# Optimization experiments

Hardware: AMD Instinct MI355X
Metric: run time of the kernel (lower is better)

The kernel has to match this reference:

```python
import jax, jax.numpy as jnp
import numpy as np

HEADS = 8


def setup_inputs() -> dict:
    key = jax.random.key(0)
    ks = jax.random.split(key, 7)
    B, C, H, W = 8, 512, 64, 64
    K, MEM = 64, 512
    s = 0.02
    return {
        "x": jax.random.normal(ks[0], (B, C, H, W), dtype=jnp.float32),
        "Ft": jax.random.normal(ks[1], (B, K, MEM), dtype=jnp.float32),
        "Wq": jax.random.normal(ks[2], (C, C), dtype=jnp.float32) * s,
        "Wk": jax.random.normal(ks[3], (C, MEM), dtype=jnp.float32) * s,
        "Wv": jax.random.normal(ks[4], (C, MEM), dtype=jnp.float32) * s,
        "Wp": jax.random.normal(ks[5], (C, C), dtype=jnp.float32) * s,
        "bp": jax.random.normal(ks[6], (C,), dtype=jnp.float32) * s,
    }


def reference(x, Ft, Wq, Wk, Wv, Wp, bp):
    B, C, H, W = x.shape
    h = HEADS
    d = C // h
    N = H * W
    # 1x1 conv query projection: (out_c, in_c) applied over spatial dims
    q = jnp.einsum('oc,bchw->bohw', Wq, x).reshape(B, h, d, N)
    q = jnp.transpose(q, (0, 1, 3, 2))                      # [B,h,N,d]
    # Linear K/V on memory tokens: Ft [B,K,MEM] @ W^T -> [B,K,C]
    k = (Ft @ Wk.T).reshape(B, -1, h, d).transpose(0, 2, 1, 3)  # [B,h,K,d]
    v = (Ft @ Wv.T).reshape(B, -1, h, d).transpose(0, 2, 1, 3)  # [B,h,K,d]
    attn = jnp.einsum('bhnc,bhkc->bhnk', q, k) / jnp.sqrt(jnp.float32(d))
    attn = jax.nn.softmax(attn, axis=-1)
    out = jnp.einsum('bhnk,bhkc->bhnc', attn, v)            # [B,h,N,d]
    out = jnp.transpose(out, (0, 1, 3, 2)).reshape(B, C, H, W)
    out = jnp.einsum('oc,bchw->bohw', Wp, out) + bp[None, :, None, None]
    return x + out
```

## Files before the change

### kernel.cpp

```cpp
#include <hip/hip_runtime.h>
#include <cstdint>
#include <cstddef>

#define BATCH 8
#define CDIM  512
#define NPIX  4096
#define NHEAD 8
#define DH    64
#define KTOK  64
#define MEM   512

#define BK    64

typedef __attribute__((ext_vector_type(8))) short          bf8;
typedef __attribute__((ext_vector_type(4))) float          f4;
typedef __attribute__((ext_vector_type(4))) unsigned short us4;

__device__ __forceinline__ unsigned short f2bf(float f){
  union { float f; unsigned int u; } x; x.f = f;
  unsigned int r = (x.u + 0x7fffu + ((x.u >> 16) & 1u)) >> 16;
  return (unsigned short)r;
}

__device__ __forceinline__ void gld_lds16(const unsigned short* g, unsigned short* lds){
  __builtin_amdgcn_global_load_lds((const __attribute__((address_space(1))) unsigned int*)g,
                                   (__attribute__((address_space(3))) unsigned int*)lds, 16, 0, 0);
}

__global__ __launch_bounds__(256) void wconv(const float* __restrict__ wq, const float* __restrict__ wp,
                                             unsigned short* __restrict__ wqb, unsigned short* __restrict__ wpb){
  int i = (blockIdx.x * 256 + threadIdx.x) * 4;
  float4 a = *(const float4*)(wq + i);
  us4 pa = { f2bf(a.x), f2bf(a.y), f2bf(a.z), f2bf(a.w) };
  *(us4*)(wqb + i) = pa;
  float4 b = *(const float4*)(wp + i);
  us4 pb = { f2bf(b.x), f2bf(b.y), f2bf(b.z), f2bf(b.w) };
  *(us4*)(wpb + i) = pb;
}

__global__ __launch_bounds__(256) void xtrans(const float* __restrict__ x, unsigned short* __restrict__ xb){
  __shared__ __align__(16) unsigned short t[64 * 68];
  int tid = threadIdx.x;
  int n0 = blockIdx.x * 64, c0 = blockIdx.y * 64, b = blockIdx.z;
  const float* xp = x + ((size_t)(b * CDIM + c0)) * NPIX + n0;
#pragma unroll
  for (int it = 0; it < 4; ++it){
    int idx = it * 1024 + tid * 4;
    int cc = idx >> 6, nn = idx & 63;
    float4 v = *(const float4*)(xp + (size_t)cc * NPIX + nn);
    us4 pk = { f2bf(v.x), f2bf(v.y), f2bf(v.z), f2bf(v.w) };
    *(us4*)&t[cc * 68 + nn] = pk;
  }
  __syncthreads();
  unsigned short* op = xb + ((size_t)(b * NPIX + n0)) * CDIM + c0;
#pragma unroll
  for (int it = 0; it < 4; ++it){
    int idx = it * 1024 + tid * 4;
    int nn = idx >> 6, c4 = idx & 63;
    us4 pk = { t[(c4 + 0) * 68 + nn], t[(c4 + 1) * 68 + nn],
               t[(c4 + 2) * 68 + nn], t[(c4 + 3) * 68 + nn] };
    *(us4*)(op + (size_t)nn * CDIM + c4) = pk;
  }
}

__global__ __launch_bounds__(256) void kvproj(const float* __restrict__ Ft, const float* __restrict__ Wk,
                                              const float* __restrict__ Wv, unsigned short* __restrict__ kb,
                                              unsigned short* __restrict__ vt){
  __shared__ float ft[8][MEM];
  int tid = threadIdx.x;
  int cg = blockIdx.x, kk0 = blockIdx.y * 8, b = blockIdx.z;
  const float* fp = Ft + ((size_t)(b * KTOK + kk0)) * MEM;
#pragma unroll
  for (int it = 0; it < 4; ++it){
    int idx = it * 1024 + tid * 4;
    int row = idx >> 9, m = idx & 511;
    *(float4*)&ft[row][m] = *(const float4*)(fp + (size_t)row * MEM + m);
  }
  __syncthreads();
  int kv = tid >> 7, cl = tid & 127;
  int c = cg * 128 + cl;
  const float* wrow = (kv ? Wv : Wk) + (size_t)c * MEM;
  float acc[8] = {0.f,0.f,0.f,0.f,0.f,0.f,0.f,0.f};
  for (int m = 0; m < MEM; m += 4){
    float4 wv4 = *(const float4*)(wrow + m);
#pragma unroll
    for (int kk = 0; kk < 8; ++kk){
      acc[kk] += wv4.x * ft[kk][m] + wv4.y * ft[kk][m+1] + wv4.z * ft[kk][m+2] + wv4.w * ft[kk][m+3];
    }
  }
  int h = c >> 6, dd = c & 63;
  if (kv == 0){
#pragma unroll
    for (int kk = 0; kk < 8; ++kk)
      kb[(((size_t)(b * NHEAD + h)) * KTOK + kk0 + kk) * DH + dd] = f2bf(acc[kk] * 0.125f);
  } else {
#pragma unroll
    for (int kk = 0; kk < 8; ++kk)
      vt[(((size_t)(b * NHEAD + h)) * DH + dd) * KTOK + kk0 + kk] = f2bf(acc[kk]);
  }
}

__global__ __launch_bounds__(256, 3) void qattn(const unsigned short* __restrict__ wqb,
                                                const unsigned short* __restrict__ xb,
                                                const unsigned short* __restrict__ kb,
                                                const unsigned short* __restrict__ vt,
                                                unsigned short* __restrict__ att){
  __shared__ __align__(16) unsigned short ab[16384];
  int tid = threadIdx.x;
  int w = tid >> 6, l = tid & 63;
  int lo = l & 15, hi = l >> 4;
  int n0 = blockIdx.x * 128, o0 = blockIdx.y * 128, b = blockIdx.z;
  int ol = (w >> 1) * 64, nl = (w & 1) * 64;

  f4 z = {0.f, 0.f, 0.f, 0.f};
  f4 accq[4][4];
#pragma unroll
  for (int i = 0; i < 4; ++i)
#pragma unroll
    for (int j = 0; j < 4; ++j) accq[i][j] = z;

  const int lrow = l >> 3;
  const int lcc  = (l & 7) ^ lrow;
  const unsigned short* asrc = wqb + ((size_t)(o0 + w * 8 + lrow)) * CDIM + lcc * 8;
  const unsigned short* bsrc = xb + ((size_t)(b * NPIX + n0 + w * 8 + lrow)) * CDIM + lcc * 8;

  for (int t = 0; t < 8; ++t){
    int kc = t * BK;
#pragma unroll
    for (int j = 0; j < 4; ++j){
      int g = j * 4 + w;
      gld_lds16(asrc + (size_t)j * 32 * CDIM + kc, &ab[g * 512]);
      gld_lds16(bsrc + (size_t)j * 32 * CDIM + kc, &ab[8192 + g * 512]);
    }
    __syncthreads();
#pragma unroll
    for (int ks = 0; ks < 2; ++ks){
      int cc = ks * 4 + hi;
      int sw = ((cc ^ (lo & 7)) << 3);
      bf8 af[4], bfr[4];
#pragma unroll
      for (int fi = 0; fi < 4; ++fi)
        af[fi] = *(const bf8*)&ab[(ol + fi * 16 + lo) * 64 + sw];
#pragma unroll
      for (int fj = 0; fj < 4; ++fj)
        bfr[fj] = *(const bf8*)&ab[8192 + (nl + fj * 16 + lo) * 64 + sw];
#pragma unroll
      for (int fi = 0; fi < 4; ++fi)
#pragma unroll
        for (int fj = 0; fj < 4; ++fj)
          accq[fi][fj] = __builtin_amdgcn_mfma_f32_16x16x32_bf16(af[fi], bfr[fj], accq[fi][fj], 0, 0, 0);
    }
    __syncthreads();
  }

  unsigned short* qt = &ab[w * 4096];
#pragma unroll
  for (int fi = 0; fi < 4; ++fi)
#pragma unroll
    for (int fj = 0; fj < 4; ++fj){
      f4 v = accq[fi][fj];
      us4 pk = { f2bf(v[0]), f2bf(v[1]), f2bf(v[2]), f2bf(v[3]) };
      int row = fj * 16 + lo;
      int col = fi * 16 + hi * 4;
      int cs  = (((col >> 3) ^ (row & 7)) << 3) | (col & 7);
      *(us4*)&qt[row * 64 + cs] = pk;
    }

  int head = blockIdx.y * 2 + (w >> 1);
  const unsigned short* kh = kb + ((size_t)(b * NHEAD + head)) * (KTOK * DH);
  f4 accs[4][4];
#pragma unroll
  for (int i = 0; i < 4; ++i)
#pragma unroll
    for (int j = 0; j < 4; ++j) accs[i][j] = z;
#pragma unroll
  for (int ks = 0; ks < 2; ++ks){
    int sw = (((ks * 4 + hi) ^ (lo & 7)) << 3);
    bf8 ka[4];
#pragma unroll
    for (int fi = 0; fi < 4; ++fi)
      ka[fi] = *(const bf8*)(kh + (fi * 16 + lo) * 64 + ks * 32 + hi * 8);
#pragma unroll
    for (int fj = 0; fj < 4; ++fj){
      bf8 qf = *(const bf8*)&qt[(fj * 16 + lo) * 64 + sw];
#pragma unroll
      for (int fi = 0; fi < 4; ++fi)
        accs[fi][fj] = __builtin_amdgcn_mfma_f32_16x16x32_bf16(ka[fi], qf, accs[fi][fj], 0, 0, 0);
    }
  }

#pragma unroll
  for (int fj = 0; fj < 4; ++fj){
    float mx = accs[0][fj][0];
#pragma unroll
    for (int fi = 0; fi < 4; ++fi)
#pragma unroll
      for (int r = 0; r < 4; ++r) mx = fmaxf(mx, accs[fi][fj][r]);
    mx = fmaxf(mx, __shfl_xor(mx, 16));
    mx = fmaxf(mx, __shfl_xor(mx, 32));
    float sm = 0.f;
#pragma unroll
    for (int fi = 0; fi < 4; ++fi)
#pragma unroll
      for (int r = 0; r < 4; ++r){
        float e = __expf(accs[fi][fj][r] - mx);
        accs[fi][fj][r] = e; sm += e;
      }
    sm += __shfl_xor(sm, 16);
    sm += __shfl_xor(sm, 32);
    float inv = 1.0f / sm;
#pragma unroll
    for (int fi = 0; fi < 4; ++fi){
      us4 pk = { f2bf(accs[fi][fj][0] * inv), f2bf(accs[fi][fj][1] * inv),
                 f2bf(accs[fi][fj][2] * inv), f2bf(accs[fi][fj][3] * inv) };
      int row = fj * 16 + lo;
      int col = fi * 16 + hi * 4;
      int cs  = (((col >> 3) ^ (row & 7)) << 3) | (col & 7);
      *(us4*)&qt[row * 64 + cs] = pk;
    }
  }

  const unsigned short* vh = vt + ((size_t)(b * NHEAD + head)) * (DH * KTOK);
  f4 acco[4][4];
#pragma unroll
  for (int i = 0; i < 4; ++i)
#pragma unroll
    for (int j = 0; j < 4; ++j) acco[i][j] = z;
#pragma unroll
  for (int ks = 0; ks < 2; ++ks){
    int sw = (((ks * 4 + hi) ^ (lo & 7)) << 3);
    bf8 va[4];
#pragma unroll
    for (int fi = 0; fi < 4; ++fi)
      va[fi] = *(const bf8*)(vh + (fi * 16 + lo) * 64 + ks * 32 + hi * 8);
#pragma unroll
    for (int fj = 0; fj < 4; ++fj){
      bf8 pf = *(const bf8*)&qt[(fj * 16 + lo) * 64 + sw];
#pragma unroll
      for (int fi = 0; fi < 4; ++fi)
        acco[fi][fj] = __builtin_amdgcn_mfma_f32_16x16x32_bf16(va[fi], pf, acco[fi][fj], 0, 0, 0);
    }
  }

  unsigned short* op = att + ((size_t)(b * NPIX + n0 + nl)) * CDIM + head * 64;
#pragma unroll
  for (int fi = 0; fi < 4; ++fi)
#pragma unroll
    for (int fj = 0; fj < 4; ++fj){
      f4 v = acco[fi][fj];
      us4 pk = { f2bf(v[0]), f2bf(v[1]), f2bf(v[2]), f2bf(v[3]) };
      *(us4*)(op + (size_t)(fj * 16 + lo) * CDIM + fi * 16 + hi * 4) = pk;
    }
}

__global__ __launch_bounds__(256, 3) void pproj(const unsigned short* __restrict__ wpb,
                                                const unsigned short* __restrict__ att,
                                                const float* __restrict__ x,
                                                const float* __restrict__ bpv,
                                                float* __restrict__ out){
  __shared__ __align__(16) unsigned short ab[16384];
  int tid = threadIdx.x;
  int w = tid >> 6, l = tid & 63;
  int lo = l & 15, hi = l >> 4;
  int n0 = blockIdx.x * 128, o0 = blockIdx.y * 128, b = blockIdx.z;
  int ol = (w >> 1) * 64, nl = (w & 1) * 64;

  f4 z = {0.f, 0.f, 0.f, 0.f};
  f4 acc[4][4];
#pragma unroll
  for (int i = 0; i < 4; ++i)
#pragma unroll
    for (int j = 0; j < 4; ++j) acc[i][j] = z;

  const int lrow = l >> 3;
  const int lcc  = (l & 7) ^ lrow;
  const unsigned short* asrc = wpb + ((size_t)(o0 + w * 8 + lrow)) * CDIM + lcc * 8;
  const unsigned short* bsrc = att + ((size_t)(b * NPIX + n0 + w * 8 + lrow)) * CDIM + lcc * 8;

  for (int t = 0; t < 8; ++t){
    int kc = t * BK;
#pragma unroll
    for (int j = 0; j < 4; ++j){
      int g = j * 4 + w;
      gld_lds16(asrc + (size_t)j * 32 * CDIM + kc, &ab[g * 512]);
      gld_lds16(bsrc + (size_t)j * 32 * CDIM + kc, &ab[8192 + g * 512]);
    }
    __syncthreads();
#pragma unroll
    for (int ks = 0; ks < 2; ++ks){
      int cc = ks * 4 + hi;
      int sw = ((cc ^ (lo & 7)) << 3);
      bf8 af[4], bfr[4];
#pragma unroll
      for (int fi = 0; fi < 4; ++fi)
        af[fi] = *(const bf8*)&ab[(ol + fi * 16 + lo) * 64 + sw];
#pragma unroll
      for (int fj = 0; fj < 4; ++fj)
        bfr[fj] = *(const bf8*)&ab[8192 + (nl + fj * 16 + lo) * 64 + sw];
#pragma unroll
      for (int fi = 0; fi < 4; ++fi)
#pragma unroll
        for (int fj = 0; fj < 4; ++fj)
          acc[fi][fj] = __builtin_amdgcn_mfma_f32_16x16x32_bf16(af[fi], bfr[fj], acc[fi][fj], 0, 0, 0);
    }
    __syncthreads();
  }

#pragma unroll
  for (int fi = 0; fi < 4; ++fi)
#pragma unroll
    for (int fj = 0; fj < 4; ++fj){
      int o = o0 + ol + fi * 16 + hi * 4;
      int n = n0 + nl + fj * 16 + lo;
#pragma unroll
      for (int r = 0; r < 4; ++r){
        size_t idx = ((size_t)(b * CDIM + o + r)) * NPIX + n;
        out[idx] = acc[fi][fj][r] + bpv[o + r] + x[idx];
      }
    }
}

extern "C" void kernel_launch(void* const* d_in, const int* in_sizes, int n_in,
                              void* d_out, int out_size, void* d_ws, size_t ws_size,
                              hipStream_t stream){
  const float* x  = (const float*)d_in[0];
  const float* Ft = (const float*)d_in[1];
  const float* Wq = (const float*)d_in[2];
  const float* Wk = (const float*)d_in[3];
  const float* Wv = (const float*)d_in[4];
  const float* Wp = (const float*)d_in[5];
  const float* bp = (const float*)d_in[6];
  float* out = (float*)d_out;

  char* ws = (char*)d_ws;
  unsigned short* wqb = (unsigned short*)(ws);
  unsigned short* wpb = (unsigned short*)(ws + 524288);
  unsigned short* xb  = (unsigned short*)(ws + 1048576);
  unsigned short* att = (unsigned short*)(ws + 1048576 + 33554432);
  unsigned short* kb  = (unsigned short*)(ws + 1048576 + 2ull * 33554432);
  unsigned short* vt  = (unsigned short*)(ws + 1048576 + 2ull * 33554432 + 524288);

  wconv<<<dim3(256), dim3(256), 0, stream>>>(Wq, Wp, wqb, wpb);
  xtrans<<<dim3(64, 8, 8), dim3(256), 0, stream>>>(x, xb);
  kvproj<<<dim3(4, 8, 8), dim3(256), 0, stream>>>(Ft, Wk, Wv, kb, vt);
  qattn<<<dim3(32, 4, 8), dim3(256), 0, stream>>>(wqb, xb, kb, vt, att);
  pproj<<<dim3(32, 4, 8), dim3(256), 0, stream>>>(wpb, att, x, bp, out);
}
```

Measured before the change: 115.7 us.

## Split Q-projection from attention and double-buffer GEMM LDS staging

Splits the fused Q-projection+attention kernel into a standalone Q GEMM that writes bf16 Q to global memory and a separate attention kernel that reads it back. Both GEMMs now use a BK=32 double-buffered LDS pipeline that prefetches the next tile while computing the current one, and occupancy hints rise from 3 to 4. The attention kernel writes its output in place over the Q buffer. This trades an extra 32 MB round trip of Q plus one more launch for better GEMM overlap and occupancy.

```diff
diff --git a/kernel.cpp b/kernel.cpp
--- a/kernel.cpp
+++ b/kernel.cpp
@@ -9,8 +9,6 @@
 #define DH    64
 #define KTOK  64
 #define MEM   512
-
-#define BK    64
 
 typedef __attribute__((ext_vector_type(8))) short          bf8;
 typedef __attribute__((ext_vector_type(4))) float          f4;
@@ -100,11 +98,44 @@
   }
 }
 
-__global__ __launch_bounds__(256, 3) void qattn(const unsigned short* __restrict__ wqb,
+#define GEMM_PRE(APTR, BPTR)                                                              \
+  const int arow = l >> 2;                                                                \
+  const int achk = (l & 3) ^ (arow & 3);                                                  \
+  const unsigned short* aS = (APTR) + (size_t)(o0 + w * 16 + arow) * CDIM + achk * 8;     \
+  const unsigned short* bS = (BPTR) + ((size_t)(b * NPIX) + n0 + w * 16 + arow) * CDIM + achk * 8;
+
+#define STAGE(p, kc)                                                                      \
+  {                                                                                       \
+    _Pragma("unroll")                                                                     \
+    for (int j = 0; j < 2; ++j){                                                          \
+      gld_lds16(aS + (size_t)j * 64 * CDIM + (kc), &ab[(p) * 8192 + (w + j * 4) * 512]);  \
+      gld_lds16(bS + (size_t)j * 64 * CDIM + (kc), &ab[(p) * 8192 + 4096 + (w + j * 4) * 512]); \
+    }                                                                                     \
+  }
+
+#define GEMM_STEP(p, ACC)                                                                 \
+  {                                                                                       \
+    bf8 af[4], bfr[4];                                                                    \
+    _Pragma("unroll")                                                                     \
+    for (int fi = 0; fi < 4; ++fi){                                                       \
+      int r = ol + fi * 16 + lo;                                                          \
+      af[fi] = *(const bf8*)&ab[(p) * 8192 + r * 32 + ((hi ^ (r & 3)) << 3)];             \
+    }                                                                                     \
+    _Pragma("unroll")                                                                     \
+    for (int fj = 0; fj < 4; ++fj){                                                       \
+      int r = nl + fj * 16 + lo;                                                          \
+      bfr[fj] = *(const bf8*)&ab[(p) * 8192 + 4096 + r * 32 + ((hi ^ (r & 3)) << 3)];     \
+    }                                                                                     \
+    _Pragma("unroll")                                                                     \
+    for (int fi = 0; fi < 4; ++fi)                                                        \
+      _Pragma("unroll")                                                                   \
+      for (int fj = 0; fj < 4; ++fj)                                                      \
+        ACC[fi][fj] = __builtin_amdgcn_mfma_f32_16x16x32_bf16(af[fi], bfr[fj], ACC[fi][fj], 0, 0, 0); \
+  }
+
+__global__ __launch_bounds__(256, 4) void qgemm(const unsigned short* __restrict__ wqb,
                                                 const unsigned short* __restrict__ xb,
-                                                const unsigned short* __restrict__ kb,
-                                                const unsigned short* __restrict__ vt,
-                                                unsigned short* __restrict__ att){
+                                                unsigned short* __restrict__ qb){
   __shared__ __align__(16) unsigned short ab[16384];
   int tid = threadIdx.x;
   int w = tid >> 6, l = tid & 63;
@@ -113,61 +144,52 @@
   int ol = (w >> 1) * 64, nl = (w & 1) * 64;
 
   f4 z = {0.f, 0.f, 0.f, 0.f};
-  f4 accq[4][4];
+  f4 acc[4][4];
 #pragma unroll
   for (int i = 0; i < 4; ++i)
 #pragma unroll
-    for (int j = 0; j < 4; ++j) accq[i][j] = z;
-
-  const int lrow = l >> 3;
-  const int lcc  = (l & 7) ^ lrow;
-  const unsigned short* asrc = wqb + ((size_t)(o0 + w * 8 + lrow)) * CDIM + lcc * 8;
-  const unsigned short* bsrc = xb + ((size_t)(b * NPIX + n0 + w * 8 + lrow)) * CDIM + lcc * 8;
-
-  for (int t = 0; t < 8; ++t){
-    int kc = t * BK;
-#pragma unroll
-    for (int j = 0; j < 4; ++j){
-      int g = j * 4 + w;
-      gld_lds16(asrc + (size_t)j * 32 * CDIM + kc, &ab[g * 512]);
-      gld_lds16(bsrc + (size_t)j * 32 * CDIM + kc, &ab[8192 + g * 512]);
-    }
+    for (int j = 0; j < 4; ++j) acc[i][j] = z;
+
+  GEMM_PRE(wqb, xb)
+
+  STAGE(0, 0)
+  __syncthreads();
+  int cur = 0;
+  for (int t = 0; t < 16; ++t){
+    if (t < 15) STAGE(cur ^ 1, (t + 1) * 32)
+    GEMM_STEP(cur, acc)
     __syncthreads();
-#pragma unroll
-    for (int ks = 0; ks < 2; ++ks){
-      int cc = ks * 4 + hi;
-      int sw = ((cc ^ (lo & 7)) << 3);
-      bf8 af[4], bfr[4];
-#pragma unroll
-      for (int fi = 0; fi < 4; ++fi)
-        af[fi] = *(const bf8*)&ab[(ol + fi * 16 + lo) * 64 + sw];
-#pragma unroll
-      for (int fj = 0; fj < 4; ++fj)
-        bfr[fj] = *(const bf8*)&ab[8192 + (nl + fj * 16 + lo) * 64 + sw];
-#pragma unroll
-      for (int fi = 0; fi < 4; ++fi)
-#pragma unroll
-        for (int fj = 0; fj < 4; ++fj)
-          accq[fi][fj] = __builtin_amdgcn_mfma_f32_16x16x32_bf16(af[fi], bfr[fj], accq[fi][fj], 0, 0, 0);
-    }
-    __syncthreads();
-  }
-
-  unsigned short* qt = &ab[w * 4096];
+    cur ^= 1;
+  }
+
+  unsigned short* op = qb + ((size_t)(b * NPIX) + n0 + nl) * CDIM + o0 + ol;
 #pragma unroll
   for (int fi = 0; fi < 4; ++fi)
 #pragma unroll
     for (int fj = 0; fj < 4; ++fj){
-      f4 v = accq[fi][fj];
+      f4 v = acc[fi][fj];
       us4 pk = { f2bf(v[0]), f2bf(v[1]), f2bf(v[2]), f2bf(v[3]) };
-      int row = fj * 16 + lo;
-      int col = fi * 16 + hi * 4;
-      int cs  = (((col >> 3) ^ (row & 7)) << 3) | (col & 7);
-      *(us4*)&qt[row * 64 + cs] = pk;
-    }
-
-  int head = blockIdx.y * 2 + (w >> 1);
-  const unsigned short* kh = kb + ((size_t)(b * NHEAD + head)) * (KTOK * DH);
+      *(us4*)(op + (size_t)(fj * 16 + lo) * CDIM + fi * 16 + hi * 4) = pk;
+    }
+}
+
+__global__ __launch_bounds__(256, 4) void attn(const unsigned short* __restrict__ qb,
+                                               const unsigned short* __restrict__ kb,
+                                               const unsigned short* __restrict__ vt,
+                                               unsigned short* __restrict__ att){
+  __shared__ __align__(16) unsigned short pb[16384];
+  int tid = threadIdx.x;
+  int w = tid >> 6, l = tid & 63;
+  int lo = l & 15, hi = l >> 4;
+  int n0 = blockIdx.x * 256 + w * 64;
+  int head = blockIdx.y, b = blockIdx.z;
+
+  const unsigned short* qh = qb + ((size_t)(b * NPIX) + n0) * CDIM + head * 64;
+  const unsigned short* kh = kb + (size_t)(b * NHEAD + head) * (KTOK * DH);
+  const unsigned short* vh = vt + (size_t)(b * NHEAD + head) * (DH * KTOK);
+  unsigned short* P = &pb[w * 4096];
+
+  f4 z = {0.f, 0.f, 0.f, 0.f};
   f4 accs[4][4];
 #pragma unroll
   for (int i = 0; i < 4; ++i)
@@ -175,14 +197,13 @@
     for (int j = 0; j < 4; ++j) accs[i][j] = z;
 #pragma unroll
   for (int ks = 0; ks < 2; ++ks){
-    int sw = (((ks * 4 + hi) ^ (lo & 7)) << 3);
     bf8 ka[4];
 #pragma unroll
     for (int fi = 0; fi < 4; ++fi)
       ka[fi] = *(const bf8*)(kh + (fi * 16 + lo) * 64 + ks * 32 + hi * 8);
 #pragma unroll
     for (int fj = 0; fj < 4; ++fj){
-      bf8 qf = *(const bf8*)&qt[(fj * 16 + lo) * 64 + sw];
+      bf8 qf = *(const bf8*)(qh + (size_t)(fj * 16 + lo) * CDIM + ks * 32 + hi * 8);
 #pragma unroll
       for (int fi = 0; fi < 4; ++fi)
         accs[fi][fj] = __builtin_amdgcn_mfma_f32_16x16x32_bf16(ka[fi], qf, accs[fi][fj], 0, 0, 0);
@@ -216,11 +237,10 @@
       int row = fj * 16 + lo;
       int col = fi * 16 + hi * 4;
       int cs  = (((col >> 3) ^ (row & 7)) << 3) | (col & 7);
-      *(us4*)&qt[row * 64 + cs] = pk;
-    }
-  }
-
-  const unsigned short* vh = vt + ((size_t)(b * NHEAD + head)) * (DH * KTOK);
+      *(us4*)&P[row * 64 + cs] = pk;
+    }
+  }
+
   f4 acco[4][4];
 #pragma unroll
   for (int i = 0; i < 4; ++i)
@@ -235,14 +255,14 @@
       va[fi] = *(const bf8*)(vh + (fi * 16 + lo) * 64 + ks * 32 + hi * 8);
 #pragma unroll
     for (int fj = 0; fj < 4; ++fj){
-      bf8 pf = *(const bf8*)&qt[(fj * 16 + lo) * 64 + sw];
+      bf8 pf = *(const bf8*)&P[(fj * 16 + lo) * 64 + sw];
 #pragma unroll
       for (int fi = 0; fi < 4; ++fi)
         acco[fi][fj] = __builtin_amdgcn_mfma_f32_16x16x32_bf16(va[fi], pf, acco[fi][fj], 0, 0, 0);
     }
   }
 
-  unsigned short* op = att + ((size_t)(b * NPIX + n0 + nl)) * CDIM + head * 64;
+  unsigned short* op = att + ((size_t)(b * NPIX) + n0) * CDIM + head * 64;
 #pragma unroll
   for (int fi = 0; fi < 4; ++fi)
 #pragma unroll
@@ -253,7 +273,7 @@
     }
 }
 
-__global__ __launch_bounds__(256, 3) void pproj(const unsigned short* __restrict__ wpb,
+__global__ __launch_bounds__(256, 4) void pproj(const unsigned short* __restrict__ wpb,
                                                 const unsigned short* __restrict__ att,
                                                 const float* __restrict__ x,
                                                 const float* __restrict__ bpv,
@@ -272,38 +292,16 @@
 #pragma unroll
     for (int j = 0; j < 4; ++j) acc[i][j] = z;
 
-  const int lrow = l >> 3;
-  const int lcc  = (l & 7) ^ lrow;
-  const unsigned short* asrc = wpb + ((size_t)(o0 + w * 8 + lrow)) * CDIM + lcc * 8;
-  const unsigned short* bsrc = att + ((size_t)(b * NPIX + n0 + w * 8 + lrow)) * CDIM + lcc * 8;
-
-  for (int t = 0; t < 8; ++t){
-    int kc = t * BK;
-#pragma unroll
-    for (int j = 0; j < 4; ++j){
-      int g = j * 4 + w;
-      gld_lds16(asrc + (size_t)j * 32 * CDIM + kc, &ab[g * 512]);
-      gld_lds16(bsrc + (size_t)j * 32 * CDIM + kc, &ab[8192 + g * 512]);
-    }
+  GEMM_PRE(wpb, att)
+
+  STAGE(0, 0)
+  __syncthreads();
+  int cur = 0;
+  for (int t = 0; t < 16; ++t){
+    if (t < 15) STAGE(cur ^ 1, (t + 1) * 32)
+    GEMM_STEP(cur, acc)
     __syncthreads();
-#pragma unroll
-    for (int ks = 0; ks < 2; ++ks){
-      int cc = ks * 4 + hi;
-      int sw = ((cc ^ (lo & 7)) << 3);
-      bf8 af[4], bfr[4];
-#pragma unroll
-      for (int fi = 0; fi < 4; ++fi)
-        af[fi] = *(const bf8*)&ab[(ol + fi * 16 + lo) * 64 + sw];
-#pragma unroll
-      for (int fj = 0; fj < 4; ++fj)
-        bfr[fj] = *(const bf8*)&ab[8192 + (nl + fj * 16 + lo) * 64 + sw];
-#pragma unroll
-      for (int fi = 0; fi < 4; ++fi)
-#pragma unroll
-        for (int fj = 0; fj < 4; ++fj)
-          acc[fi][fj] = __builtin_amdgcn_mfma_f32_16x16x32_bf16(af[fi], bfr[fj], acc[fi][fj], 0, 0, 0);
-    }
-    __syncthreads();
+    cur ^= 1;
   }
 
 #pragma unroll
@@ -336,13 +334,14 @@
   unsigned short* wqb = (unsigned short*)(ws);
   unsigned short* wpb = (unsigned short*)(ws + 524288);
   unsigned short* xb  = (unsigned short*)(ws + 1048576);
-  unsigned short* att = (unsigned short*)(ws + 1048576 + 33554432);
+  unsigned short* qb  = (unsigned short*)(ws + 1048576 + 33554432);
   unsigned short* kb  = (unsigned short*)(ws + 1048576 + 2ull * 33554432);
   unsigned short* vt  = (unsigned short*)(ws + 1048576 + 2ull * 33554432 + 524288);
 
   wconv<<<dim3(256), dim3(256), 0, stream>>>(Wq, Wp, wqb, wpb);
   xtrans<<<dim3(64, 8, 8), dim3(256), 0, stream>>>(x, xb);
   kvproj<<<dim3(4, 8, 8), dim3(256), 0, stream>>>(Ft, Wk, Wv, kb, vt);
-  qattn<<<dim3(32, 4, 8), dim3(256), 0, stream>>>(wqb, xb, kb, vt, att);
-  pproj<<<dim3(32, 4, 8), dim3(256), 0, stream>>>(wpb, att, x, bp, out);
-}
+  qgemm<<<dim3(32, 4, 8), dim3(256), 0, stream>>>(wqb, xb, qb);
+  attn<<<dim3(16, 8, 8), dim3(256), 0, stream>>>(qb, kb, vt, qb);
+  pproj<<<dim3(32, 4, 8), dim3(256), 0, stream>>>(wpb, qb, x, bp, out);
+}
```

Measured after the change: 132.8 us. 14.7% more time.

## Fuse query projection, attention and output projection into one kernel

Applied to the files above, without the earlier changes.

Merges the qattn and pproj kernels into one 512-thread kernel. Each block covers all 512 output channels for 128 pixels, with one wave per head. The attention output stays in LDS instead of making a 32MB bf16 round trip through global memory, and the separate output-projection launch goes away. In exchange, weights are read directly from global memory with no LDS staging, the grid drops to 256 blocks, and register pressure is high (accq[4][8] plus further accumulators), which risks lower occupancy and spills.

```diff
diff --git a/kernel.cpp b/kernel.cpp
--- a/kernel.cpp
+++ b/kernel.cpp
@@ -9,8 +9,6 @@
 #define DH    64
 #define KTOK  64
 #define MEM   512
-
-#define BK    64
 
 typedef __attribute__((ext_vector_type(8))) short          bf8;
 typedef __attribute__((ext_vector_type(4))) float          f4;
@@ -100,224 +98,197 @@
   }
 }
 
-__global__ __launch_bounds__(256, 3) void qattn(const unsigned short* __restrict__ wqb,
+__global__ __launch_bounds__(512, 2) void fused(const unsigned short* __restrict__ wqb,
+                                                const unsigned short* __restrict__ wpb,
                                                 const unsigned short* __restrict__ xb,
                                                 const unsigned short* __restrict__ kb,
                                                 const unsigned short* __restrict__ vt,
-                                                unsigned short* __restrict__ att){
-  __shared__ __align__(16) unsigned short ab[16384];
+                                                const float* __restrict__ x,
+                                                const float* __restrict__ bpv,
+                                                float* __restrict__ out){
+  __shared__ __align__(16) unsigned short r0[32768];
+  __shared__ __align__(16) unsigned short r1[32768];
   int tid = threadIdx.x;
   int w = tid >> 6, l = tid & 63;
   int lo = l & 15, hi = l >> 4;
-  int n0 = blockIdx.x * 128, o0 = blockIdx.y * 128, b = blockIdx.z;
-  int ol = (w >> 1) * 64, nl = (w & 1) * 64;
+  int n0 = blockIdx.x * 128, b = blockIdx.y;
 
   f4 z = {0.f, 0.f, 0.f, 0.f};
-  f4 accq[4][4];
+
+  f4 accq[4][8];
 #pragma unroll
   for (int i = 0; i < 4; ++i)
 #pragma unroll
-    for (int j = 0; j < 4; ++j) accq[i][j] = z;
-
-  const int lrow = l >> 3;
-  const int lcc  = (l & 7) ^ lrow;
-  const unsigned short* asrc = wqb + ((size_t)(o0 + w * 8 + lrow)) * CDIM + lcc * 8;
-  const unsigned short* bsrc = xb + ((size_t)(b * NPIX + n0 + w * 8 + lrow)) * CDIM + lcc * 8;
+    for (int j = 0; j < 8; ++j) accq[i][j] = z;
+
+  const int srow = l >> 3;
+  const int schk = (l & 7) ^ srow;
+  const unsigned short* bS = xb + ((size_t)(b * NPIX) + n0 + w * 8 + srow) * CDIM + schk * 8;
+  const unsigned short* aQ = wqb + (size_t)(w * 64 + lo) * CDIM + hi * 8;
 
   for (int t = 0; t < 8; ++t){
-    int kc = t * BK;
-#pragma unroll
-    for (int j = 0; j < 4; ++j){
-      int g = j * 4 + w;
-      gld_lds16(asrc + (size_t)j * 32 * CDIM + kc, &ab[g * 512]);
-      gld_lds16(bsrc + (size_t)j * 32 * CDIM + kc, &ab[8192 + g * 512]);
-    }
+    gld_lds16(bS + t * 64, &r0[w * 512]);
+    gld_lds16(bS + (size_t)64 * CDIM + t * 64, &r0[(w + 8) * 512]);
     __syncthreads();
 #pragma unroll
     for (int ks = 0; ks < 2; ++ks){
-      int cc = ks * 4 + hi;
-      int sw = ((cc ^ (lo & 7)) << 3);
-      bf8 af[4], bfr[4];
-#pragma unroll
-      for (int fi = 0; fi < 4; ++fi)
-        af[fi] = *(const bf8*)&ab[(ol + fi * 16 + lo) * 64 + sw];
-#pragma unroll
-      for (int fj = 0; fj < 4; ++fj)
-        bfr[fj] = *(const bf8*)&ab[8192 + (nl + fj * 16 + lo) * 64 + sw];
-#pragma unroll
-      for (int fi = 0; fi < 4; ++fi)
-#pragma unroll
-        for (int fj = 0; fj < 4; ++fj)
+      bf8 af[4], bfr[8];
+#pragma unroll
+      for (int fi = 0; fi < 4; ++fi)
+        af[fi] = *(const bf8*)(aQ + (size_t)fi * 16 * CDIM + t * 64 + ks * 32);
+#pragma unroll
+      for (int fj = 0; fj < 8; ++fj)
+        bfr[fj] = *(const bf8*)&r0[(fj * 16 + lo) * 64 + (((ks * 4 + hi) ^ (lo & 7)) << 3)];
+#pragma unroll
+      for (int fi = 0; fi < 4; ++fi)
+#pragma unroll
+        for (int fj = 0; fj < 8; ++fj)
           accq[fi][fj] = __builtin_amdgcn_mfma_f32_16x16x32_bf16(af[fi], bfr[fj], accq[fi][fj], 0, 0, 0);
     }
     __syncthreads();
   }
 
-  unsigned short* qt = &ab[w * 4096];
-#pragma unroll
-  for (int fi = 0; fi < 4; ++fi)
-#pragma unroll
-    for (int fj = 0; fj < 4; ++fj){
-      f4 v = accq[fi][fj];
-      us4 pk = { f2bf(v[0]), f2bf(v[1]), f2bf(v[2]), f2bf(v[3]) };
-      int row = fj * 16 + lo;
-      int col = fi * 16 + hi * 4;
-      int cs  = (((col >> 3) ^ (row & 7)) << 3) | (col & 7);
-      *(us4*)&qt[row * 64 + cs] = pk;
-    }
-
-  int head = blockIdx.y * 2 + (w >> 1);
-  const unsigned short* kh = kb + ((size_t)(b * NHEAD + head)) * (KTOK * DH);
-  f4 accs[4][4];
-#pragma unroll
-  for (int i = 0; i < 4; ++i)
-#pragma unroll
-    for (int j = 0; j < 4; ++j) accs[i][j] = z;
-#pragma unroll
-  for (int ks = 0; ks < 2; ++ks){
-    int sw = (((ks * 4 + hi) ^ (lo & 7)) << 3);
-    bf8 ka[4];
+  const unsigned short* kh = kb + (size_t)(b * NHEAD + w) * (KTOK * DH);
+  const unsigned short* vh = vt + (size_t)(b * NHEAD + w) * (DH * KTOK);
+  unsigned short* qt = &r0[w * 4096];
+
+#pragma unroll
+  for (int nh = 0; nh < 2; ++nh){
 #pragma unroll
     for (int fi = 0; fi < 4; ++fi)
-      ka[fi] = *(const bf8*)(kh + (fi * 16 + lo) * 64 + ks * 32 + hi * 8);
-#pragma unroll
-    for (int fj = 0; fj < 4; ++fj){
-      bf8 qf = *(const bf8*)&qt[(fj * 16 + lo) * 64 + sw];
-#pragma unroll
-      for (int fi = 0; fi < 4; ++fi)
-        accs[fi][fj] = __builtin_amdgcn_mfma_f32_16x16x32_bf16(ka[fi], qf, accs[fi][fj], 0, 0, 0);
-    }
-  }
-
-#pragma unroll
-  for (int fj = 0; fj < 4; ++fj){
-    float mx = accs[0][fj][0];
+#pragma unroll
+      for (int fjl = 0; fjl < 4; ++fjl){
+        f4 v = accq[fi][nh * 4 + fjl];
+        us4 pk = { f2bf(v[0]), f2bf(v[1]), f2bf(v[2]), f2bf(v[3]) };
+        int row = fjl * 16 + lo;
+        int col = fi * 16 + hi * 4;
+        int cs  = (((col >> 3) ^ (row & 7)) << 3) | (col & 7);
+        *(us4*)&qt[row * 64 + cs] = pk;
+      }
+
+    f4 accs[4][4];
+#pragma unroll
+    for (int i = 0; i < 4; ++i)
+#pragma unroll
+      for (int j = 0; j < 4; ++j) accs[i][j] = z;
+#pragma unroll
+    for (int ks = 0; ks < 2; ++ks){
+      bf8 ka[4];
+#pragma unroll
+      for (int fi = 0; fi < 4; ++fi)
+        ka[fi] = *(const bf8*)(kh + (fi * 16 + lo) * 64 + ks * 32 + hi * 8);
+#pragma unroll
+      for (int fjl = 0; fjl < 4; ++fjl){
+        bf8 qf = *(const bf8*)&qt[(fjl * 16 + lo) * 64 + (((ks * 4 + hi) ^ (lo & 7)) << 3)];
+#pragma unroll
+        for (int fi = 0; fi < 4; ++fi)
+          accs[fi][fjl] = __builtin_amdgcn_mfma_f32_16x16x32_bf16(ka[fi], qf, accs[fi][fjl], 0, 0, 0);
+      }
+    }
+
+#pragma unroll
+    for (int fjl = 0; fjl < 4; ++fjl){
+      float mx = accs[0][fjl][0];
+#pragma unroll
+      for (int fi = 0; fi < 4; ++fi)
+#pragma unroll
+        for (int r = 0; r < 4; ++r) mx = fmaxf(mx, accs[fi][fjl][r]);
+      mx = fmaxf(mx, __shfl_xor(mx, 16));
+      mx = fmaxf(mx, __shfl_xor(mx, 32));
+      float sm = 0.f;
+#pragma unroll
+      for (int fi = 0; fi < 4; ++fi)
+#pragma unroll
+        for (int r = 0; r < 4; ++r){
+          float e = __expf(accs[fi][fjl][r] - mx);
+          accs[fi][fjl][r] = e; sm += e;
+        }
+      sm += __shfl_xor(sm, 16);
+      sm += __shfl_xor(sm, 32);
+      float inv = 1.0f / sm;
+#pragma unroll
+      for (int fi = 0; fi < 4; ++fi){
+        us4 pk = { f2bf(accs[fi][fjl][0] * inv), f2bf(accs[fi][fjl][1] * inv),
+                   f2bf(accs[fi][fjl][2] * inv), f2bf(accs[fi][fjl][3] * inv) };
+        int row = fjl * 16 + lo;
+        int col = fi * 16 + hi * 4;
+        int cs  = (((col >> 3) ^ (row & 7)) << 3) | (col & 7);
+        *(us4*)&qt[row * 64 + cs] = pk;
+      }
+    }
+
+    f4 acco[4][4];
+#pragma unroll
+    for (int i = 0; i < 4; ++i)
+#pragma unroll
+      for (int j = 0; j < 4; ++j) acco[i][j] = z;
+#pragma unroll
+    for (int ks = 0; ks < 2; ++ks){
+      int sw = (((ks * 4 + hi) ^ (lo & 7)) << 3);
+      bf8 va[4];
+#pragma unroll
+      for (int fi = 0; fi < 4; ++fi)
+        va[fi] = *(const bf8*)(vh + (fi * 16 + lo) * 64 + ks * 32 + hi * 8);
+#pragma unroll
+      for (int fjl = 0; fjl < 4; ++fjl){
+        bf8 pf = *(const bf8*)&qt[(fjl * 16 + lo) * 64 + sw];
+#pragma unroll
+        for (int fi = 0; fi < 4; ++fi)
+          acco[fi][fjl] = __builtin_amdgcn_mfma_f32_16x16x32_bf16(va[fi], pf, acco[fi][fjl], 0, 0, 0);
+      }
+    }
+
+    __syncthreads();
 #pragma unroll
     for (int fi = 0; fi < 4; ++fi)
 #pragma unroll
-      for (int r = 0; r < 4; ++r) mx = fmaxf(mx, accs[fi][fj][r]);
-    mx = fmaxf(mx, __shfl_xor(mx, 16));
-    mx = fmaxf(mx, __shfl_xor(mx, 32));
-    float sm = 0.f;
+      for (int fjl = 0; fjl < 4; ++fjl){
+        f4 v = acco[fi][fjl];
+        us4 pk = { f2bf(v[0]), f2bf(v[1]), f2bf(v[2]), f2bf(v[3]) };
+        int row = fjl * 16 + lo;
+        int cc  = w * 8 + fi * 2 + (hi >> 1);
+        *(us4*)&r1[row * 512 + ((cc ^ (row & 7)) << 3) + (hi & 1) * 4] = pk;
+      }
+    __syncthreads();
+
+    f4 accp[4][4];
+#pragma unroll
+    for (int i = 0; i < 4; ++i)
+#pragma unroll
+      for (int j = 0; j < 4; ++j) accp[i][j] = z;
+    const unsigned short* aP = wpb + (size_t)(w * 64 + lo) * CDIM + hi * 8;
+#pragma unroll
+    for (int t = 0; t < 8; ++t){
+#pragma unroll
+      for (int ks = 0; ks < 2; ++ks){
+        bf8 pa[4], bt[4];
+#pragma unroll
+        for (int fi = 0; fi < 4; ++fi)
+          pa[fi] = *(const bf8*)(aP + (size_t)fi * 16 * CDIM + t * 64 + ks * 32);
+#pragma unroll
+        for (int fjl = 0; fjl < 4; ++fjl)
+          bt[fjl] = *(const bf8*)&r1[(fjl * 16 + lo) * 512 + (((t * 8 + ks * 4 + hi) ^ (lo & 7)) << 3)];
+#pragma unroll
+        for (int fi = 0; fi < 4; ++fi)
+#pragma unroll
+          for (int fjl = 0; fjl < 4; ++fjl)
+            accp[fi][fjl] = __builtin_amdgcn_mfma_f32_16x16x32_bf16(pa[fi], bt[fjl], accp[fi][fjl], 0, 0, 0);
+      }
+    }
+
 #pragma unroll
     for (int fi = 0; fi < 4; ++fi)
 #pragma unroll
-      for (int r = 0; r < 4; ++r){
-        float e = __expf(accs[fi][fj][r] - mx);
-        accs[fi][fj][r] = e; sm += e;
-      }
-    sm += __shfl_xor(sm, 16);
-    sm += __shfl_xor(sm, 32);
-    float inv = 1.0f / sm;
-#pragma unroll
-    for (int fi = 0; fi < 4; ++fi){
-      us4 pk = { f2bf(accs[fi][fj][0] * inv), f2bf(accs[fi][fj][1] * inv),
-                 f2bf(accs[fi][fj][2] * inv), f2bf(accs[fi][fj][3] * inv) };
-      int row = fj * 16 + lo;
-      int col = fi * 16 + hi * 4;
-      int cs  = (((col >> 3) ^ (row & 7)) << 3) | (col & 7);
-      *(us4*)&qt[row * 64 + cs] = pk;
-    }
-  }
-
-  const unsigned short* vh = vt + ((size_t)(b * NHEAD + head)) * (DH * KTOK);
-  f4 acco[4][4];
-#pragma unroll
-  for (int i = 0; i < 4; ++i)
-#pragma unroll
-    for (int j = 0; j < 4; ++j) acco[i][j] = z;
-#pragma unroll
-  for (int ks = 0; ks < 2; ++ks){
-    int sw = (((ks * 4 + hi) ^ (lo & 7)) << 3);
-    bf8 va[4];
-#pragma unroll
-    for (int fi = 0; fi < 4; ++fi)
-      va[fi] = *(const bf8*)(vh + (fi * 16 + lo) * 64 + ks * 32 + hi * 8);
-#pragma unroll
-    for (int fj = 0; fj < 4; ++fj){
-      bf8 pf = *(const bf8*)&qt[(fj * 16 + lo) * 64 + sw];
-#pragma unroll
-      for (int fi = 0; fi < 4; ++fi)
-        acco[fi][fj] = __builtin_amdgcn_mfma_f32_16x16x32_bf16(va[fi], pf, acco[fi][fj], 0, 0, 0);
-    }
-  }
-
-  unsigned short* op = att + ((size_t)(b * NPIX + n0 + nl)) * CDIM + head * 64;
-#pragma unroll
-  for (int fi = 0; fi < 4; ++fi)
-#pragma unroll
-    for (int fj = 0; fj < 4; ++fj){
-      f4 v = acco[fi][fj];
-      us4 pk = { f2bf(v[0]), f2bf(v[1]), f2bf(v[2]), f2bf(v[3]) };
-      *(us4*)(op + (size_t)(fj * 16 + lo) * CDIM + fi * 16 + hi * 4) = pk;
-    }
-}
-
-__global__ __launch_bounds__(256, 3) void pproj(const unsigned short* __restrict__ wpb,
-                                                const unsigned short* __restrict__ att,
-                                                const float* __restrict__ x,
-                                                const float* __restrict__ bpv,
-                                                float* __restrict__ out){
-  __shared__ __align__(16) unsigned short ab[16384];
-  int tid = threadIdx.x;
-  int w = tid >> 6, l = tid & 63;
-  int lo = l & 15, hi = l >> 4;
-  int n0 = blockIdx.x * 128, o0 = blockIdx.y * 128, b = blockIdx.z;
-  int ol = (w >> 1) * 64, nl = (w & 1) * 64;
-
-  f4 z = {0.f, 0.f, 0.f, 0.f};
-  f4 acc[4][4];
-#pragma unroll
-  for (int i = 0; i < 4; ++i)
-#pragma unroll
-    for (int j = 0; j < 4; ++j) acc[i][j] = z;
-
-  const int lrow = l >> 3;
-  const int lcc  = (l & 7) ^ lrow;
-  const unsigned short* asrc = wpb + ((size_t)(o0 + w * 8 + lrow)) * CDIM + lcc * 8;
-  const unsigned short* bsrc = att + ((size_t)(b * NPIX + n0 + w * 8 + lrow)) * CDIM + lcc * 8;
-
-  for (int t = 0; t < 8; ++t){
-    int kc = t * BK;
-#pragma unroll
-    for (int j = 0; j < 4; ++j){
-      int g = j * 4 + w;
-      gld_lds16(asrc + (size_t)j * 32 * CDIM + kc, &ab[g * 512]);
-      gld_lds16(bsrc + (size_t)j * 32 * CDIM + kc, &ab[8192 + g * 512]);
-    }
-    __syncthreads();
-#pragma unroll
-    for (int ks = 0; ks < 2; ++ks){
-      int cc = ks * 4 + hi;
-      int sw = ((cc ^ (lo & 7)) << 3);
-      bf8 af[4], bfr[4];
-#pragma unroll
-      for (int fi = 0; fi < 4; ++fi)
-        af[fi] = *(const bf8*)&ab[(ol + fi * 16 + lo) * 64 + sw];
-#pragma unroll
-      for (int fj = 0; fj < 4; ++fj)
-        bfr[fj] = *(const bf8*)&ab[8192 + (nl + fj * 16 + lo) * 64 + sw];
-#pragma unroll
-      for (int fi = 0; fi < 4; ++fi)
-#pragma unroll
-        for (int fj = 0; fj < 4; ++fj)
-          acc[fi][fj] = __builtin_amdgcn_mfma_f32_16x16x32_bf16(af[fi], bfr[fj], acc[fi][fj], 0, 0, 0);
-    }
-    __syncthreads();
-  }
-
-#pragma unroll
-  for (int fi = 0; fi < 4; ++fi)
-#pragma unroll
-    for (int fj = 0; fj < 4; ++fj){
-      int o = o0 + ol + fi * 16 + hi * 4;
-      int n = n0 + nl + fj * 16 + lo;
-#pragma unroll
-      for (int r = 0; r < 4; ++r){
-        size_t idx = ((size_t)(b * CDIM + o + r)) * NPIX + n;
-        out[idx] = acc[fi][fj][r] + bpv[o + r] + x[idx];
-      }
-    }
+      for (int fjl = 0; fjl < 4; ++fjl){
+        int o = w * 64 + fi * 16 + hi * 4;
+        int n = n0 + nh * 64 + fjl * 16 + lo;
+#pragma unroll
+        for (int r = 0; r < 4; ++r){
+          size_t idx = ((size_t)(b * CDIM + o + r)) * NPIX + n;
+          out[idx] = accp[fi][fjl][r] + bpv[o + r] + x[idx];
+        }
+      }
+  }
 }
 
 extern "C" void kernel_launch(void* const* d_in, const int* in_sizes, int n_in,
@@ -336,13 +307,11 @@
   unsigned short* wqb = (unsigned short*)(ws);
   unsigned short* wpb = (unsigned short*)(ws + 524288);
   unsigned short* xb  = (unsigned short*)(ws + 1048576);
-  unsigned short* att = (unsigned short*)(ws + 1048576 + 33554432);
-  unsigned short* kb  = (unsigned short*)(ws + 1048576 + 2ull * 33554432);
-  unsigned short* vt  = (unsigned short*)(ws + 1048576 + 2ull * 33554432 + 524288);
+  unsigned short* kb  = (unsigned short*)(ws + 1048576 + 33554432);
+  unsigned short* vt  = (unsigned short*)(ws + 1048576 + 33554432 + 524288);
 
   wconv<<<dim3(256), dim3(256), 0, stream>>>(Wq, Wp, wqb, wpb);
   xtrans<<<dim3(64, 8, 8), dim3(256), 0, stream>>>(x, xb);
   kvproj<<<dim3(4, 8, 8), dim3(256), 0, stream>>>(Ft, Wk, Wv, kb, vt);
-  qattn<<<dim3(32, 4, 8), dim3(256), 0, stream>>>(wqb, xb, kb, vt, att);
-  pproj<<<dim3(32, 4, 8), dim3(256), 0, stream>>>(wpb, att, x, bp, out);
-}
+  fused<<<dim3(32, 8), dim3(512), 0, stream>>>(wqb, wpb, xb, kb, vt, x, bp, out);
+}
```

After: 142.3 us. 22.9% more time.
